# Kernel tuning notes

Measured on AMD Instinct MI355X. Metric: run time of the kernel, lower is better.

## Reference

```python
import jax, jax.numpy as jnp
import numpy as np

# SRM neuron constants (match init_kwargs)
THRESH = 0.3
TAU_M = 16.0
TAU_S = 4.0
DT = 1.0
LENS = 0.5
DECAY_M = float(np.exp(-DT / TAU_M))
DECAY_S = float(np.exp(-DT / TAU_S))

B, T = 16, 16
SHAPES = [(B, 64, 64, 64), (B, 128, 64, 64), (B, 128, 32, 32), (B, 512), (B, 11)]


@jax.custom_vjp
def spike_fn(u):
    # Heaviside spike with rectangular surrogate gradient (width 2*lens),
    # the smooth-math stand-in for the LUT-based grad_u_approx.
    return (u > THRESH).astype(u.dtype)

def _spike_fwd(u):
    return spike_fn(u), u

def _spike_bwd(u, g):
    surr = (jnp.abs(u - THRESH) < LENS).astype(u.dtype) / (2.0 * LENS)
    return (g * surr,)

spike_fn.defvjp(_spike_fwd, _spike_bwd)


def conv(x, w):
    # 3x3 conv, stride 1, padding 1, no bias (NCHW / OIHW)
    return jax.lax.conv_general_dilated(x, w, (1, 1), [(1, 1), (1, 1)],
                                        dimension_numbers=('NCHW', 'OIHW', 'NCHW'))


def maxpool2(x):
    return jax.lax.reduce_window(x, -jnp.inf, jax.lax.max, (1, 1, 2, 2), (1, 1, 2, 2), 'VALID')


def srm_update(I, vm, vs, s_prev):
    # SRM dynamics: two exponential traces (LUT exp decay in original),
    # reset via previous spike, membrane potential u = vm - vs.
    vm = DECAY_M * vm * (1.0 - s_prev) + I
    vs = DECAY_S * vs * (1.0 - s_prev) + I
    s = spike_fn(vm - vs)
    return vm, vs, s


def _xavier(key, shape):
    if len(shape) == 4:  # OIHW conv
        fan_in = shape[1] * shape[2] * shape[3]
        fan_out = shape[0] * shape[2] * shape[3]
    else:  # Linear [out, in]
        fan_in, fan_out = shape[1], shape[0]
    lim = float(np.sqrt(6.0 / (fan_in + fan_out)))
    return jax.random.uniform(key, shape, jnp.float32, -lim, lim)


def setup_inputs() -> dict:
    key = jax.random.key(0)
    ks = jax.random.split(key, 6)
    inp = jax.random.uniform(ks[0], (B, T, 2, 64, 64), jnp.float32)
    return {
        'input': inp,
        'W0': _xavier(ks[1], (64, 2, 3, 3)),
        'W1': _xavier(ks[2], (128, 64, 3, 3)),
        'W2': _xavier(ks[3], (128, 128, 3, 3)),
        'W3': _xavier(ks[4], (512, 32768)),
        'W4': _xavier(ks[5], (11, 512)),
        'batch_size': B,
        'num_steps': T,
    }


def reference(input, W0, W1, W2, W3, W4, batch_size, num_steps):
    x = jnp.transpose(input, (1, 0, 2, 3, 4))  # [T, B, 2, 64, 64]
    z = lambda s: jnp.zeros(s, jnp.float32)
    vm = tuple(z(s) for s in SHAPES)
    vs = tuple(z(s) for s in SHAPES)
    sp = tuple(z(s) for s in SHAPES)
    out_sum = z((batch_size, 11))

    def step(carry, xt):
        vm, vs, sp, out_sum = carry
        in_spike = jnp.clip(xt, 0.0, 1.0)  # limit == 'yes'
        vm0, vs0, s0 = srm_update(conv(in_spike, W0), vm[0], vs[0], sp[0])
        vm1, vs1, s1 = srm_update(conv(s0, W1), vm[1], vs[1], sp[1])
        p1 = maxpool2(s1)                                    # [B,128,32,32]
        vm2, vs2, s2 = srm_update(conv(p1, W2), vm[2], vs[2], sp[2])
        p2 = maxpool2(s2).reshape(batch_size, -1)            # [B, 32768]
        vm3, vs3, s3 = srm_update(p2 @ W3.T, vm[3], vs[3], sp[3])
        vm4, vs4, s4 = srm_update(s3 @ W4.T, vm[4], vs[4], sp[4])
        new_carry = ((vm0, vm1, vm2, vm3, vm4), (vs0, vs1, vs2, vs3, vs4),
                     (s0, s1, s2, s3, s4), out_sum + s4)
        return new_carry, None

    (_, _, _, out_sum), _ = jax.lax.scan(step, (vm, vs, sp, out_sum), x)
    return out_sum / num_steps
```

## Files before the change

### kernel.cpp

```cpp
#include <hip/hip_runtime.h>
#include <hip/hip_bf16.h>
#include <math.h>

#define DM 0.9394130628134758f
#define DSC 0.7788007830714049f
#define TH 0.3f

#define B 16
#define T 16

typedef short short8 __attribute__((ext_vector_type(8)));
typedef float f32x4 __attribute__((ext_vector_type(4)));
typedef int i32x4 __attribute__((ext_vector_type(4)));

__device__ __forceinline__ void srm(float& m, float& s, float p, float I, float& spk) {
    m = DM * m * (1.f - p) + I;
    s = DSC * s * (1.f - p) + I;
    spk = (m - s > TH) ? 1.f : 0.f;
}

__global__ __launch_bounds__(256) void k_prep_i8(const float* __restrict__ W,
                                                 signed char* __restrict__ Wd,
                                                 int CO, int CI,
                                                 float s1, float s2, float s3) {
    int idx = blockIdx.x * 256 + threadIdx.x;
    int total = CO * CI * 9;
    if (idx >= total) return;
    int tap = idx % 9, tmp = idx / 9, ci = tmp % CI, co = tmp / CI;
    float w = W[((size_t)co * CI + ci) * 9 + tap];
    float d1 = rintf(w / s1);
    float r1 = fmaf(-d1, s1, w);
    float d2 = rintf(r1 / s2);
    float r2 = fmaf(-d2, s2, r1);
    float d3 = rintf(r2 / s3);
    d1 = fminf(fmaxf(d1, -127.f), 127.f);
    d2 = fminf(fmaxf(d2, -127.f), 127.f);
    d3 = fminf(fmaxf(d3, -127.f), 127.f);
    size_t base = ((size_t)tap * CO + co) * CI + ci;
    size_t stride = (size_t)9 * CO * CI;
    Wd[base] = (signed char)(int)d1;
    Wd[base + stride] = (signed char)(int)d2;
    Wd[base + 2 * stride] = (signed char)(int)d3;
}

__global__ __launch_bounds__(256) void k_prep3(const float* __restrict__ W3,
                                               unsigned short* __restrict__ W3p) {
    int bid = blockIdx.x;
    int ot = bid >> 8, ks4 = bid & 255;
    int lane = threadIdx.x & 63, wv = threadIdx.x >> 6;
    int kstep = ks4 * 4 + wv;
    int n = lane & 15, q = lane >> 4;
    const float* src = W3 + (size_t)(ot * 16 + n) * 32768 + kstep * 32 + q * 8;
    float4 w0 = *(const float4*)src;
    float4 w1 = *(const float4*)(src + 4);
    float wj[8] = {w0.x, w0.y, w0.z, w0.w, w1.x, w1.y, w1.z, w1.w};
    short8 hh, mm, ll;
#pragma unroll
    for (int j = 0; j < 8; j++) {
        __hip_bfloat16 h = __float2bfloat16(wj[j]);
        float hf = __bfloat162float(h);
        __hip_bfloat16 m = __float2bfloat16(wj[j] - hf);
        float mf = __bfloat162float(m);
        __hip_bfloat16 l = __float2bfloat16(wj[j] - hf - mf);
        hh[j] = *(short*)&h; mm[j] = *(short*)&m; ll[j] = *(short*)&l;
    }
    size_t pos = (((size_t)ot * 1024 + kstep) * 64 + lane) * 8;
    *(short8*)(W3p + pos) = hh;
    *(short8*)(W3p + 16777216 + pos) = mm;
    *(short8*)(W3p + 33554432 + pos) = ll;
}

#define S0 68
__global__ __launch_bounds__(128) void k_conv0T(const float* __restrict__ in,
                                                const float* __restrict__ W0,
                                                signed char* __restrict__ s0b) {
    __shared__ float tile[2][10 * S0];
    int bid = blockIdx.x;
    int cog = bid & 7, yt = (bid >> 3) & 7, b = bid >> 6;
    int tid = threadIdx.x;
    int tx = (tid & 15) * 4, ty = tid >> 4;
    int y0 = yt * 8, y = y0 + ty;

    float m[8][4] = {}, s[8][4] = {};
    unsigned pmask = 0;

    for (int t = 0; t < T; t++) {
        if (t) __syncthreads();
        for (int i = tid; i < 2 * 660; i += 128) {
            int cl = i / 660, rem = i - cl * 660;
            int r = rem / 66, c = rem - r * 66;
            int gy = y0 + r - 1, gx = c - 1;
            float v = 0.f;
            if ((unsigned)gy < 64u && (unsigned)gx < 64u) {
                const float* src = in + ((size_t)((b * T + t) * 2 + cl)) * 4096;
                v = fminf(fmaxf(src[gy * 64 + gx], 0.f), 1.f);
            }
            tile[cl][r * S0 + c] = v;
        }
        __syncthreads();

        float acc[8][4] = {};
#pragma unroll
        for (int cl = 0; cl < 2; cl++) {
            const float* wb = W0 + ((size_t)cog * 8 * 2 + cl) * 9;
#pragma unroll
            for (int dy = 0; dy < 3; dy++) {
                float4 A = *(const float4*)&tile[cl][(ty + dy) * S0 + tx];
                float4 Bv = *(const float4*)&tile[cl][(ty + dy) * S0 + tx + 4];
                float r0 = A.x, r1 = A.y, r2 = A.z, r3 = A.w, r4 = Bv.x, r5 = Bv.y;
#pragma unroll
                for (int c = 0; c < 8; c++) {
                    const float* w = wb + (size_t)c * 2 * 9 + dy * 3;
                    float wa = w[0], wbx = w[1], wc = w[2];
                    acc[c][0] += wa * r0 + wbx * r1 + wc * r2;
                    acc[c][1] += wa * r1 + wbx * r2 + wc * r3;
                    acc[c][2] += wa * r2 + wbx * r3 + wc * r4;
                    acc[c][3] += wa * r3 + wbx * r4 + wc * r5;
                }
            }
        }

        unsigned newmask = 0;
        signed char* s0p = s0b + ((size_t)(t * 16 + b) * 4096) * 64;
#pragma unroll
        for (int j = 0; j < 4; j++) {
            unsigned long long vv = 0ULL;
#pragma unroll
            for (int c = 0; c < 8; c++) {
                int bit = c * 4 + j;
                float p = (pmask >> bit) & 1 ? 1.f : 0.f;
                float spk;
                srm(m[c][j], s[c][j], p, acc[c][j], spk);
                bool on = spk > 0.5f;
                if (on) { newmask |= 1u << bit; vv |= 1ULL << (8 * c); }
            }
            *(unsigned long long*)(s0p + ((size_t)(y * 64 + tx + j)) * 64 + cog * 8) = vv;
        }
        pmask = newmask;
    }
}

__global__ __launch_bounds__(512, 2) void k_conv1T(const signed char* __restrict__ s0b,
                                                   const signed char* __restrict__ W1d,
                                                   signed char* __restrict__ p1b,
                                                   float s1, float s2, float s3) {
    __shared__ i32x4 atile[1360];
    __shared__ i32x4 wlds[3456];
    int bid = blockIdx.x;
    int b = bid & 15;
    int rest = bid >> 4;
    int cg = rest & 3;
    int xh = (rest >> 2) & 1;
    int yq = rest >> 3;
    int tid = threadIdx.x;
    int lane = tid & 63, wv = tid >> 6;
    int cog_l = wv >> 2, rq = wv & 3;
    int n = lane & 15, q = lane >> 4;
    int y0 = yq * 8;

    const i32x4 zf = {0, 0, 0, 0};
    for (int i = tid; i < 1360; i += 512) atile[i] = zf;
    for (int idx = tid; idx < 3456; idx += 512) {
        int qq = idx & 3, nn = (idx >> 2) & 15;
        int r27 = (idx >> 6) % 27, cl = idx / 1728;
        int tm = r27 % 3, tap = r27 / 3;
        int dst = (idx & ~3) | ((qq + (nn >> 1)) & 3);
        wlds[dst] = *(const i32x4*)(W1d +
            ((size_t)(tm * 9 + tap) * 128 + cg * 32 + cl * 16 + nn) * 64 + qq * 16);
    }

    int off_[3], ldsi_[3];
    bool ok_[3];
#pragma unroll
    for (int j = 0; j < 3; j++) {
        ok_[j] = false; ldsi_[j] = 0; off_[j] = 0;
        int item = tid + j * 512;
        if (item < 1360) {
            int r = item / 136, rem = item - r * 136;
            int xl = rem >> 2, c = rem & 3;
            ldsi_[j] = (r * 34 + xl) * 4 + ((c + (xl >> 1)) & 3);
            int gy = y0 - 1 + r;
            int gx = xh * 32 + xl - 1;
            if ((unsigned)gy < 64u && (unsigned)gx < 64u) {
                ok_[j] = true;
                off_[j] = (gy * 64 + gx) * 64 + c * 16;
            }
        }
    }
    __syncthreads();

    {
        const signed char* sb = s0b + ((size_t)(0 * 16 + b) * 4096) * 64;
#pragma unroll
        for (int j = 0; j < 3; j++)
            if (ok_[j]) atile[ldsi_[j]] = *(const i32x4*)(sb + off_[j]);
    }
    __syncthreads();

    int xp_s = lane >> 2, cq = lane & 3;
    int xt_s = xp_s >> 3, q_s = (xp_s >> 1) & 3, rp_s = xp_s & 1;

    int cbase_w = cog_l * 1728;
    float sm[4][4] = {}, ss[4][4] = {};
    unsigned pmask = 0;

    for (int t = 0; t < T; t++) {
        i32x4 pf0 = zf, pf1 = zf, pf2 = zf;
        bool pfv = (t + 1 < T);
        if (pfv) {
            const signed char* sb1 = s0b + ((size_t)((t + 1) * 16 + b) * 4096) * 64;
            if (ok_[0]) pf0 = *(const i32x4*)(sb1 + off_[0]);
            if (ok_[1]) pf1 = *(const i32x4*)(sb1 + off_[1]);
            if (ok_[2]) pf2 = *(const i32x4*)(sb1 + off_[2]);
        }

        i32x4 accH[4], accM[4], accL[4];
#pragma unroll
        for (int u = 0; u < 4; u++) { accH[u] = zf; accM[u] = zf; accL[u] = zf; }

#pragma unroll
        for (int dy = 0; dy < 3; dy++) {
#pragma unroll
            for (int dx = 0; dx < 3; dx++) {
                int tap = dy * 3 + dx;
                i32x4 Af[2][2];
#pragma unroll
                for (int ro = 0; ro < 2; ro++) {
                    int r = rq * 2 + ro + dy;
#pragma unroll
                    for (int xt = 0; xt < 2; xt++) {
                        int x = xt * 16 + n + dx;
                        Af[ro][xt] = atile[(r * 34 + x) * 4 + ((q + (x >> 1)) & 3)];
                    }
                }
                {
                    i32x4 Bf = wlds[cbase_w + (tap * 3 + 0) * 64 + n * 4 + ((q + (n >> 1)) & 3)];
#pragma unroll
                    for (int ro = 0; ro < 2; ro++)
#pragma unroll
                        for (int xt = 0; xt < 2; xt++)
                            accH[ro * 2 + xt] = __builtin_amdgcn_mfma_i32_16x16x64_i8(
                                Af[ro][xt], Bf, accH[ro * 2 + xt], 0, 0, 0);
                }
                {
                    i32x4 Bf = wlds[cbase_w + (tap * 3 + 1) * 64 + n * 4 + ((q + (n >> 1)) & 3)];
#pragma unroll
                    for (int ro = 0; ro < 2; ro++)
#pragma unroll
                        for (int xt = 0; xt < 2; xt++)
                            accM[ro * 2 + xt] = __builtin_amdgcn_mfma_i32_16x16x64_i8(
                                Af[ro][xt], Bf, accM[ro * 2 + xt], 0, 0, 0);
                }
                {
                    i32x4 Bf = wlds[cbase_w + (tap * 3 + 2) * 64 + n * 4 + ((q + (n >> 1)) & 3)];
#pragma unroll
                    for (int ro = 0; ro < 2; ro++)
#pragma unroll
                        for (int xt = 0; xt < 2; xt++)
                            accL[ro * 2 + xt] = __builtin_amdgcn_mfma_i32_16x16x64_i8(
                                Af[ro][xt], Bf, accL[ro * 2 + xt], 0, 0, 0);
                }
            }
        }

        unsigned newmask = 0;
#pragma unroll
        for (int ro = 0; ro < 2; ro++)
#pragma unroll
            for (int xt = 0; xt < 2; xt++)
#pragma unroll
                for (int r = 0; r < 4; r++) {
                    int u = ro * 2 + xt;
                    int bit = u * 4 + r;
                    float p = (pmask >> bit) & 1 ? 1.f : 0.f;
                    float I = fmaf((float)accH[u][r], s1,
                             fmaf((float)accM[u][r], s2, (float)accL[u][r] * s3));
                    float spk;
                    srm(sm[u][r], ss[u][r], p, I, spk);
                    if (spk > 0.5f) newmask |= 1u << bit;
                }
        pmask = newmask;

        unsigned bits4 = 0;
#pragma unroll
        for (int xt = 0; xt < 2; xt++)
#pragma unroll
            for (int rp = 0; rp < 2; rp++) {
                int i0 = (0 * 2 + xt) * 4 + 2 * rp;
                int i1 = (1 * 2 + xt) * 4 + 2 * rp;
                unsigned on = ((newmask >> i0) | (newmask >> (i0 + 1)) |
                               (newmask >> i1) | (newmask >> (i1 + 1))) & 1u;
                unsigned long long bal = __ballot(on != 0);
                if (xt == xt_s && rp == rp_s)
                    bits4 = (unsigned)(bal >> (q_s * 16 + cq * 4)) & 0xFu;
            }
        unsigned vv = (bits4 & 1u) | (((bits4 >> 1) & 1u) << 8) |
                      (((bits4 >> 2) & 1u) << 16) | (((bits4 >> 3) & 1u) << 24);
        signed char* pb = p1b + (((size_t)(t * 16 + b) * 8) + cg * 2 + cog_l) * 16384;
        int px = (yq * 4 + rq) * 32 + xh * 16 + xp_s;
        *(unsigned*)(pb + (size_t)px * 16 + cq * 4) = vv;

        __syncthreads();
        if (pfv) {
            if (ok_[0]) atile[ldsi_[0]] = pf0;
            if (ok_[1]) atile[ldsi_[1]] = pf1;
            if (ok_[2]) atile[ldsi_[2]] = pf2;
        }
        __syncthreads();
    }
}

__global__ __launch_bounds__(512, 2) void k_conv2T(const signed char* __restrict__ p1b,
                                                   const signed char* __restrict__ W2d,
                                                   unsigned short* __restrict__ p2a,
                                                   float s1, float s2, float s3) {
    __shared__ i32x4 atile[4896];
    __shared__ i32x4 wlds[3456];
    int bid = blockIdx.x;
    int xcd = bid & 7, rest = bid >> 3;
    int b = ((rest & 1) << 3) | xcd;
    int yh = (rest >> 1) & 1;
    int cog = (rest >> 2) & 7;
    int tid = threadIdx.x;
    int lane = tid & 63, wv = tid >> 6;
    int n = lane & 15, q = lane >> 4;
    int y0 = yh * 16;

    const i32x4 zf = {0, 0, 0, 0};
    for (int i = tid; i < 4896; i += 512) atile[i] = zf;
    for (int idx = tid; idx < 3456; idx += 512) {
        int c8 = idx & 7, nn = (idx >> 3) & 15, rem = idx >> 7;
        int tm = rem % 3, tap = rem / 3;
        int dst = (idx & ~7) | (c8 ^ ((nn & 1) << 2));
        wlds[dst] = *(const i32x4*)(W2d +
            ((size_t)(tm * 9 + tap) * 128 + cog * 16 + nn) * 128 + c8 * 16);
    }

    int yr = yh * 8 + wv;
    int co = cog * 16 + n;

    float sm[2][2][4] = {}, ss[2][2][4] = {};
    unsigned pmask = 0;

    for (int t = 0; t < T; t++) {
        __syncthreads();
        const signed char* sb = p1b + (((size_t)(t * 16 + b)) << 17);
        for (int i = tid; i < 4608; i += 512) {
            int c = i & 7, x32 = (i >> 3) & 31, r = i >> 8;
            int gy = y0 - 1 + r;
            if ((unsigned)gy < 32u) {
                int xtile = x32 + 1;
                atile[(r * 34 + xtile) * 8 + (c ^ ((xtile & 1) << 2))] =
                    *(const i32x4*)(sb + (((size_t)c) << 14) + ((size_t)(gy * 32 + x32)) * 16);
            }
        }
        __syncthreads();

        i32x4 accH[2][2], accM[2][2], accL[2][2];
#pragma unroll
        for (int i = 0; i < 2; i++)
#pragma unroll
            for (int j = 0; j < 2; j++) { accH[i][j] = zf; accM[i][j] = zf; accL[i][j] = zf; }

#pragma unroll
        for (int ks = 0; ks < 2; ks++) {
#pragma unroll
            for (int dy = 0; dy < 3; dy++) {
                int rA = wv * 2 + dy, rB = rA + 1;
#pragma unroll
                for (int dx = 0; dx < 3; dx++) {
                    int tap = dy * 3 + dx;
                    i32x4 AfA[2], AfB[2];
#pragma unroll
                    for (int xt = 0; xt < 2; xt++) {
                        int x = xt * 16 + n + dx;
                        int slA = (ks * 4 + q) ^ ((x & 1) << 2);
                        AfA[xt] = atile[(rA * 34 + x) * 8 + slA];
                        AfB[xt] = atile[(rB * 34 + x) * 8 + slA];
                    }
                    int slB = (ks * 4 + q) ^ ((n & 1) << 2);
                    {
                        i32x4 Bf = wlds[(tap * 3 + 0) * 128 + n * 8 + slB];
#pragma unroll
                        for (int xt = 0; xt < 2; xt++) {
                            accH[0][xt] = __builtin_amdgcn_mfma_i32_16x16x64_i8(AfA[xt], Bf, accH[0][xt], 0, 0, 0);
                            accH[1][xt] = __builtin_amdgcn_mfma_i32_16x16x64_i8(AfB[xt], Bf, accH[1][xt], 0, 0, 0);
                        }
                    }
                    {
                        i32x4 Bf = wlds[(tap * 3 + 1) * 128 + n * 8 + slB];
#pragma unroll
                        for (int xt = 0; xt < 2; xt++) {
                            accM[0][xt] = __builtin_amdgcn_mfma_i32_16x16x64_i8(AfA[xt], Bf, accM[0][xt], 0, 0, 0);
                            accM[1][xt] = __builtin_amdgcn_mfma_i32_16x16x64_i8(AfB[xt], Bf, accM[1][xt], 0, 0, 0);
                        }
                    }
                    {
                        i32x4 Bf = wlds[(tap * 3 + 2) * 128 + n * 8 + slB];
#pragma unroll
                        for (int xt = 0; xt < 2; xt++) {
                            accL[0][xt] = __builtin_amdgcn_mfma_i32_16x16x64_i8(AfA[xt], Bf, accL[0][xt], 0, 0, 0);
                            accL[1][xt] = __builtin_amdgcn_mfma_i32_16x16x64_i8(AfB[xt], Bf, accL[1][xt], 0, 0, 0);
                        }
                    }
                }
            }
        }

        unsigned newmask = 0;
#pragma unroll
        for (int yo = 0; yo < 2; yo++)
#pragma unroll
            for (int xt = 0; xt < 2; xt++)
#pragma unroll
                for (int r = 0; r < 4; r++) {
                    int bit = (yo * 2 + xt) * 4 + r;
                    float p = (pmask >> bit) & 1 ? 1.f : 0.f;
                    float I = fmaf((float)accH[yo][xt][r], s1,
                             fmaf((float)accM[yo][xt][r], s2, (float)accL[yo][xt][r] * s3));
                    float spk;
                    srm(sm[yo][xt][r], ss[yo][xt][r], p, I, spk);
                    if (spk > 0.5f) newmask |= 1u << bit;
                }
        pmask = newmask;

        int kstep = co * 8 + (yr >> 1);
        size_t base_t = ((size_t)t * 1024 + kstep) * 512;
#pragma unroll
        for (int xt = 0; xt < 2; xt++) {
            int i00 = (0 * 2 + xt) * 4 + 0, i10 = (1 * 2 + xt) * 4 + 0;
            int i01 = (0 * 2 + xt) * 4 + 2, i11 = (1 * 2 + xt) * 4 + 2;
            unsigned on0 = ((newmask >> i00) | (newmask >> (i00 + 1)) |
                            (newmask >> i10) | (newmask >> (i10 + 1))) & 1u;
            unsigned on1 = ((newmask >> i01) | (newmask >> (i01 + 1)) |
                            (newmask >> i11) | (newmask >> (i11 + 1))) & 1u;
            unsigned v32 = (on0 ? 0x3F80u : 0u) | (on1 ? 0x3F800000u : 0u);
            int qp = (yr & 1) * 2 + xt;
            *(unsigned*)(p2a + base_t + (size_t)(qp * 16 + b) * 8 + q * 2) = v32;
        }
    }
}

__global__ __launch_bounds__(256) void k_fc3(const unsigned short* __restrict__ p2a,
                                             const unsigned short* __restrict__ W3p,
                                             float* __restrict__ I3p) {
    int bid = blockIdx.x;
    int ob = bid & 7, r2 = bid >> 3;
    int t = r2 & 15, ks = r2 >> 4;
    int lane = threadIdx.x & 63, w = threadIdx.x >> 6;
    int ot = ob * 4 + w;

    const unsigned short* ap = p2a + ((size_t)t * 1024 + ks * 128) * 512 + lane * 8;
    const unsigned short* bp = W3p + ((size_t)ot * 1024 + ks * 128) * 512 + lane * 8;

    f32x4 acc = {0.f, 0.f, 0.f, 0.f};
#pragma unroll 8
    for (int kk = 0; kk < 128; kk++) {
        short8 A = *(const short8*)(ap + (size_t)kk * 512);
        short8 B0 = *(const short8*)(bp + (size_t)kk * 512);
        short8 B1 = *(const short8*)(bp + 16777216 + (size_t)kk * 512);
        short8 B2 = *(const short8*)(bp + 33554432 + (size_t)kk * 512);
        acc = __builtin_amdgcn_mfma_f32_16x16x32_bf16(A, B0, acc, 0, 0, 0);
        acc = __builtin_amdgcn_mfma_f32_16x16x32_bf16(A, B1, acc, 0, 0, 0);
        acc = __builtin_amdgcn_mfma_f32_16x16x32_bf16(A, B2, acc, 0, 0, 0);
    }
    int n = lane & 15, q = lane >> 4;
    float* op = I3p + ((size_t)(t * 8 + ks)) * 8192 + ot * 16 + n;
#pragma unroll
    for (int r = 0; r < 4; r++)
        op[(size_t)(q * 4 + r) * 512] = acc[r];
}

__global__ __launch_bounds__(256) void k_srm3T(const float* __restrict__ I3p,
                                               float* __restrict__ sp3) {
    int idx = blockIdx.x * 256 + threadIdx.x;
    float m = 0.f, s = 0.f, p = 0.f;
    for (int t = 0; t < T; t++) {
        float I = 0.f;
#pragma unroll
        for (int ks = 0; ks < 8; ks++) I += I3p[((size_t)(t * 8 + ks)) * 8192 + idx];
        float spk;
        srm(m, s, p, I, spk);
        p = spk;
        sp3[t * 8192 + idx] = spk;
    }
}

__global__ __launch_bounds__(256) void k_fc4g(const float* __restrict__ sp3,
                                              const float* __restrict__ W4,
                                              float* __restrict__ I4) {
    int t = blockIdx.x, tid = threadIdx.x;
    if (tid >= 176) return;
    int b = tid / 11, o = tid - b * 11;
    const float4* a = (const float4*)(sp3 + (size_t)t * 8192 + b * 512);
    const float4* w = (const float4*)(W4 + o * 512);
    float acc = 0.f;
    for (int k = 0; k < 128; k++) {
        float4 x = a[k], y = w[k];
        acc += x.x * y.x + x.y * y.y + x.z * y.z + x.w * y.w;
    }
    I4[(size_t)(t * 16 + b) * 11 + o] = acc;
}

__global__ __launch_bounds__(256) void k_fc4s(const float* __restrict__ I4,
                                              float* __restrict__ out) {
    int tid = threadIdx.x;
    if (tid >= 176) return;
    int b = tid / 11, o = tid - b * 11;
    float m = 0.f, s = 0.f, p = 0.f, sum = 0.f;
    for (int t = 0; t < T; t++) {
        float I = I4[(size_t)(t * 16 + b) * 11 + o];
        float spk;
        srm(m, s, p, I, spk);
        p = spk;
        sum += spk;
    }
    out[tid] = sum * 0.0625f;
}

extern "C" void kernel_launch(void* const* d_in, const int* in_sizes, int n_in,
                              void* d_out, int out_size, void* d_ws, size_t ws_size,
                              hipStream_t stream) {
    const float* in = (const float*)d_in[0];
    const float* W0 = (const float*)d_in[1];
    const float* W1 = (const float*)d_in[2];
    const float* W2 = (const float*)d_in[3];
    const float* W3 = (const float*)d_in[4];
    const float* W4 = (const float*)d_in[5];
    float* out = (float*)d_out;
    char* ws = (char*)d_ws;

    size_t off = 0;
    auto alloc = [&](size_t bytes) {
        void* p = ws + off;
        off += (bytes + 255) & ~(size_t)255;
        return p;
    };
    signed char* s0b = (signed char*)alloc((size_t)256 * 4096 * 64);
    signed char* p1b = (signed char*)alloc((size_t)256 * 1024 * 128);
    unsigned short* p2a = (unsigned short*)alloc((size_t)16 * 1024 * 512 * 2);
    float* I3p = (float*)alloc((size_t)128 * 8192 * 4);
    float* sp3 = (float*)alloc((size_t)16 * 8192 * 4);
    float* I4  = (float*)alloc((size_t)256 * 11 * 4);
    signed char* W1d = (signed char*)alloc((size_t)3 * 9 * 128 * 64);
    signed char* W2d = (signed char*)alloc((size_t)3 * 9 * 128 * 128);
    unsigned short* W3p = (unsigned short*)alloc((size_t)3 * 512 * 32768 * 2);

    double lim1 = sqrt(6.0 / (64.0 * 9 + 128.0 * 9));
    double lim2 = sqrt(6.0 / (128.0 * 9 + 128.0 * 9));
    float s1a = (float)(lim1 / 127.0);
    float s2a = s1a / 254.0f;
    float s3a = s2a / 64.0f;
    float s1b = (float)(lim2 / 127.0);
    float s2b = s1b / 254.0f;
    float s3b = s2b / 64.0f;

    k_prep_i8<<<(9 * 128 * 64 + 255) / 256, 256, 0, stream>>>(W1, W1d, 128, 64, s1a, s2a, s3a);
    k_prep_i8<<<(9 * 128 * 128 + 255) / 256, 256, 0, stream>>>(W2, W2d, 128, 128, s1b, s2b, s3b);
    k_prep3<<<8192, 256, 0, stream>>>(W3, W3p);

    k_conv0T<<<16 * 8 * 8, 128, 0, stream>>>(in, W0, s0b);
    k_conv1T<<<1024, 512, 0, stream>>>(s0b, W1d, p1b, s1a, s2a, s3a);
    k_conv2T<<<256, 512, 0, stream>>>(p1b, W2d, p2a, s1b, s2b, s3b);
    k_fc3<<<1024, 256, 0, stream>>>(p2a, W3p, I3p);
    k_srm3T<<<8192 / 256, 256, 0, stream>>>(I3p, sp3);
    k_fc4g<<<16, 256, 0, stream>>>(sp3, W4, I4);
    k_fc4s<<<1, 256, 0, stream>>>(I4, out);
}
```

Before: 783.2 us.

## Remap conv0 threads to all output channels of a small spatial tile

Result: faster. 662.1 us, median of 2 (-15.5%).

```diff
diff --git a/kernel.cpp b/kernel.cpp
--- a/kernel.cpp
+++ b/kernel.cpp
@@ -70,52 +70,59 @@
     *(short8*)(W3p + 33554432 + pos) = ll;
 }
 
-#define S0 68
-__global__ __launch_bounds__(128) void k_conv0T(const float* __restrict__ in,
+#define S0T 20
+__global__ __launch_bounds__(256) void k_conv0T(const float* __restrict__ in,
                                                 const float* __restrict__ W0,
                                                 signed char* __restrict__ s0b) {
-    __shared__ float tile[2][10 * S0];
+    __shared__ float tile[2][10][S0T];
     int bid = blockIdx.x;
-    int cog = bid & 7, yt = (bid >> 3) & 7, b = bid >> 6;
+    int b = bid & 15;
+    int rest = bid >> 4;
+    int xt = rest & 3, yt = rest >> 2;
     int tid = threadIdx.x;
-    int tx = (tid & 15) * 4, ty = tid >> 4;
-    int y0 = yt * 8, y = y0 + ty;
+    int cog = tid & 7, pxg = tid >> 3;
+    int y0 = yt * 8, x0 = xt * 16;
 
     float m[8][4] = {}, s[8][4] = {};
     unsigned pmask = 0;
 
+    const float* wb = W0 + (size_t)cog * 8 * 2 * 9;
+
     for (int t = 0; t < T; t++) {
         if (t) __syncthreads();
-        for (int i = tid; i < 2 * 660; i += 128) {
-            int cl = i / 660, rem = i - cl * 660;
-            int r = rem / 66, c = rem - r * 66;
-            int gy = y0 + r - 1, gx = c - 1;
+        for (int i = tid; i < 360; i += 256) {
+            int ci = i / 180, rem = i - ci * 180;
+            int r = rem / 18, cc = rem - r * 18;
+            int gy = y0 + r - 1, gx = x0 + cc - 1;
             float v = 0.f;
             if ((unsigned)gy < 64u && (unsigned)gx < 64u) {
-                const float* src = in + ((size_t)((b * T + t) * 2 + cl)) * 4096;
+                const float* src = in + ((size_t)((b * T + t) * 2 + ci)) * 4096;
                 v = fminf(fmaxf(src[gy * 64 + gx], 0.f), 1.f);
             }
-            tile[cl][r * S0 + c] = v;
+            tile[ci][r][cc] = v;
         }
         __syncthreads();
 
         float acc[8][4] = {};
 #pragma unroll
-        for (int cl = 0; cl < 2; cl++) {
-            const float* wb = W0 + ((size_t)cog * 8 * 2 + cl) * 9;
+        for (int ci = 0; ci < 2; ci++) {
 #pragma unroll
             for (int dy = 0; dy < 3; dy++) {
-                float4 A = *(const float4*)&tile[cl][(ty + dy) * S0 + tx];
-                float4 Bv = *(const float4*)&tile[cl][(ty + dy) * S0 + tx + 4];
-                float r0 = A.x, r1 = A.y, r2 = A.z, r3 = A.w, r4 = Bv.x, r5 = Bv.y;
-#pragma unroll
-                for (int c = 0; c < 8; c++) {
-                    const float* w = wb + (size_t)c * 2 * 9 + dy * 3;
-                    float wa = w[0], wbx = w[1], wc = w[2];
-                    acc[c][0] += wa * r0 + wbx * r1 + wc * r2;
-                    acc[c][1] += wa * r1 + wbx * r2 + wc * r3;
-                    acc[c][2] += wa * r2 + wbx * r3 + wc * r4;
-                    acc[c][3] += wa * r3 + wbx * r4 + wc * r5;
+#pragma unroll
+                for (int dx = 0; dx < 3; dx++) {
+                    float wv[8];
+#pragma unroll
+                    for (int c = 0; c < 8; c++)
+                        wv[c] = wb[((size_t)c * 2 + ci) * 9 + dy * 3 + dx];
+#pragma unroll
+                    for (int j = 0; j < 4; j++) {
+                        int px = pxg + 32 * j;
+                        int y = px >> 4, x = px & 15;
+                        float tv = tile[ci][y + dy][x + dx];
+#pragma unroll
+                        for (int c = 0; c < 8; c++)
+                            acc[c][j] += wv[c] * tv;
+                    }
                 }
             }
         }
@@ -134,7 +141,9 @@
                 bool on = spk > 0.5f;
                 if (on) { newmask |= 1u << bit; vv |= 1ULL << (8 * c); }
             }
-            *(unsigned long long*)(s0p + ((size_t)(y * 64 + tx + j)) * 64 + cog * 8) = vv;
+            int px = pxg + 32 * j;
+            int gpx = (y0 + (px >> 4)) * 64 + x0 + (px & 15);
+            *(unsigned long long*)(s0p + (size_t)gpx * 64 + cog * 8) = vv;
         }
         pmask = newmask;
     }
@@ -559,7 +568,7 @@
     k_prep_i8<<<(9 * 128 * 128 + 255) / 256, 256, 0, stream>>>(W2, W2d, 128, 128, s1b, s2b, s3b);
     k_prep3<<<8192, 256, 0, stream>>>(W3, W3p);
 
-    k_conv0T<<<16 * 8 * 8, 128, 0, stream>>>(in, W0, s0b);
+    k_conv0T<<<512, 256, 0, stream>>>(in, W0, s0b);
     k_conv1T<<<1024, 512, 0, stream>>>(s0b, W1d, p1b, s1a, s2a, s3a);
     k_conv2T<<<256, 512, 0, stream>>>(p1b, W2d, p2a, s1b, s2b, s3b);
     k_fc3<<<1024, 256, 0, stream>>>(p2a, W3p, I3p);
```
